# Performance work log

Measured on AMD Instinct MI355X. Metric: run time of the kernel, lower is better.

The kernel has to match this reference:

```python
import jax, jax.numpy as jnp
import numpy as np

V = 50000
E = 500000
D = 128


def setup_inputs() -> dict:
    key = jax.random.key(0)
    k1, k2, k3, k4, k5, k6 = jax.random.split(key, 6)
    edge_feats = jax.random.normal(k1, (E, D), dtype=jnp.float32)
    node_feats = jax.random.normal(k2, (V, 1), dtype=jnp.float32)
    edge_index = jax.random.randint(k3, (2, E), 0, V, dtype=jnp.int64)
    rev_index = jax.random.randint(k4, (E,), 0, E, dtype=jnp.int64)
    # Linear(hidden_dim, hidden_dim, bias=True) params, Kaiming-uniform-ish init
    lim = 1.0 / np.sqrt(D)
    W = jax.random.uniform(k5, (D, D), dtype=jnp.float32, minval=-lim, maxval=lim)
    b = jax.random.uniform(k6, (D,), dtype=jnp.float32, minval=-lim, maxval=lim)
    return {"edge_feats": edge_feats, "node_feats": node_feats, "W": W, "b": b,
            "edge_index": edge_index, "rev_index": rev_index}


def reference(edge_feats, node_feats, W, b, edge_index, rev_index):
    src, dest = edge_index[0], edge_index[1]
    messages = jax.nn.relu(edge_feats)                      # [E, d]
    # scatter-sum messages onto destination nodes
    node_messages = jax.ops.segment_sum(messages, dest, num_segments=node_feats.shape[0])  # [V, d]
    # gather back to edges, subtract reverse-edge message (D-MPNN)
    edge_messages = node_messages[src] - messages[rev_index]  # [E, d]
    # update: Linear (dropout p=0.0 is identity)
    return edge_messages @ W.T + b
```

## Files before the change

kernel.cpp:

```cpp
#include <hip/hip_runtime.h>

#define DD 128
#define TILE_E 64

typedef __attribute__((ext_vector_type(8))) short short8;
typedef __attribute__((ext_vector_type(4))) float f32x4;

__device__ __forceinline__ unsigned short f2bf(float f) {
  unsigned int u = __float_as_uint(f);
  u += 0x7FFF + ((u >> 16) & 1);
  return (unsigned short)(u >> 16);
}


__global__ __launch_bounds__(256) void hist_kernel(
    const int* __restrict__ eidx, int* __restrict__ cnt, int E) {
  int e = blockIdx.x * 256 + threadIdx.x;
  if (e < E) atomicAdd(&cnt[eidx[E + e]], 1);
}

__global__ __launch_bounds__(1024) void scan_kernel(
    const int* __restrict__ cnt, int* __restrict__ off, int* __restrict__ cur, int V) {
  __shared__ int s[1024];
  const int t = threadIdx.x;
  const int chunk = (V + 1023) / 1024;
  const int lo = t * chunk, hi = min(lo + chunk, V);
  int tot = 0;
  for (int v = lo; v < hi; ++v) tot += cnt[v];
  s[t] = tot;
  __syncthreads();
  for (int d = 1; d < 1024; d <<= 1) {
    int x = (t >= d) ? s[t - d] : 0;
    __syncthreads();
    s[t] += x;
    __syncthreads();
  }
  int run = (t > 0) ? s[t - 1] : 0;
  for (int v = lo; v < hi; ++v) {
    off[v] = run; cur[v] = run;
    run += cnt[v];
  }
}

__global__ __launch_bounds__(256) void fill_kernel(
    const int* __restrict__ eidx, int* __restrict__ cur,
    int* __restrict__ elist, int E) {
  int e = blockIdx.x * 256 + threadIdx.x;
  if (e < E) {
    int p = atomicAdd(&cur[eidx[E + e]], 1);
    elist[p] = e;
  }
}

__global__ __launch_bounds__(256) void gather_sum_kernel(
    const float* __restrict__ ef, const int* __restrict__ off,
    const int* __restrict__ cnt, const int* __restrict__ elist,
    float* __restrict__ nm, int V) {
  const int lane = threadIdx.x & 63;
  const int v = blockIdx.x * 4 + (threadIdx.x >> 6);
  if (v >= V) return;
  const int base = off[v];
  const int deg  = cnt[v];
  float2 acc0 = make_float2(0.f, 0.f);
  float2 acc1 = make_float2(0.f, 0.f);
  int j = 0;
  for (; j + 4 <= deg; j += 4) {
    int ea = elist[base + j + 0];
    int eb = elist[base + j + 1];
    int ec = elist[base + j + 2];
    int ed = elist[base + j + 3];
    float2 ma = ((const float2*)(ef + (size_t)ea * DD))[lane];
    float2 mb = ((const float2*)(ef + (size_t)eb * DD))[lane];
    float2 mc = ((const float2*)(ef + (size_t)ec * DD))[lane];
    float2 md = ((const float2*)(ef + (size_t)ed * DD))[lane];
    acc0.x += fmaxf(ma.x, 0.f) + fmaxf(mb.x, 0.f);
    acc0.y += fmaxf(ma.y, 0.f) + fmaxf(mb.y, 0.f);
    acc1.x += fmaxf(mc.x, 0.f) + fmaxf(md.x, 0.f);
    acc1.y += fmaxf(mc.y, 0.f) + fmaxf(md.y, 0.f);
  }
  for (; j < deg; ++j) {
    int e = elist[base + j];
    float2 m = ((const float2*)(ef + (size_t)e * DD))[lane];
    acc0.x += fmaxf(m.x, 0.f);
    acc0.y += fmaxf(m.y, 0.f);
  }
  ((float2*)(nm + (size_t)v * DD))[lane] =
      make_float2(acc0.x + acc1.x, acc0.y + acc1.y);
}

__global__ __launch_bounds__(256) void wconv_kernel(
    const float* __restrict__ W, unsigned short* __restrict__ Wswz) {
  int idx = blockIdx.x * 256 + threadIdx.x;
  if (idx >= DD * DD / 8) return;
  int lane = idx & 63;
  int nt   = (idx >> 6) & 7;
  int kt   = idx >> 9;
  int n = nt * 16 + (lane & 15);
  int k = kt * 32 + (lane >> 4) * 8;
  const float4* wrow = (const float4*)(W + (size_t)n * DD + k);
  float4 w0 = wrow[0];
  float4 w1 = wrow[1];
  unsigned int p0 = f2bf(w0.x) | ((unsigned int)f2bf(w0.y) << 16);
  unsigned int p1 = f2bf(w0.z) | ((unsigned int)f2bf(w0.w) << 16);
  unsigned int p2 = f2bf(w1.x) | ((unsigned int)f2bf(w1.y) << 16);
  unsigned int p3 = f2bf(w1.z) | ((unsigned int)f2bf(w1.w) << 16);
  ((uint4*)Wswz)[idx] = make_uint4(p0, p1, p2, p3);
}

__global__ __launch_bounds__(256, 4) void fused_gather_gemm_kernel(
    const float* __restrict__ ef, const float* __restrict__ nm,
    const unsigned short* __restrict__ Wswz, const float* __restrict__ bias,
    const int* __restrict__ eidx, const int* __restrict__ rev,
    float* __restrict__ out, int E) {
  const int tid  = threadIdx.x;
  const int lane = tid & 63;
  const int wave = tid >> 6;
  const int col  = lane & 15;
  const int quad = lane >> 4;
  const int e0   = blockIdx.x * TILE_E + wave * 16;

  const int ea = e0 + col;
  int s = 0, rv = 0;
  if (ea < E) { s = eidx[ea]; rv = rev[ea]; }
  const float4* __restrict__ nmp = (const float4*)(nm + (size_t)s  * DD);
  const float4* __restrict__ efp = (const float4*)(ef + (size_t)rv * DD);
  const short8* __restrict__ wp  = (const short8*)Wswz + lane;

  f32x4 acc[8];
  #pragma unroll
  for (int i = 0; i < 8; ++i) acc[i] = (f32x4){0.f, 0.f, 0.f, 0.f};

  #pragma unroll
  for (int kt = 0; kt < 4; ++kt) {
    const int k4 = kt * 8 + quad * 2;
    float4 a0 = nmp[k4];
    float4 a1 = nmp[k4 + 1];
    float4 m0 = efp[k4];
    float4 m1 = efp[k4 + 1];
    float x0 = a0.x - fmaxf(m0.x, 0.f);
    float x1 = a0.y - fmaxf(m0.y, 0.f);
    float x2 = a0.z - fmaxf(m0.z, 0.f);
    float x3 = a0.w - fmaxf(m0.w, 0.f);
    float x4 = a1.x - fmaxf(m1.x, 0.f);
    float x5 = a1.y - fmaxf(m1.y, 0.f);
    float x6 = a1.z - fmaxf(m1.z, 0.f);
    float x7 = a1.w - fmaxf(m1.w, 0.f);
    union { unsigned int u[4]; short8 s8; } cvt;
    cvt.u[0] = f2bf(x0) | ((unsigned int)f2bf(x1) << 16);
    cvt.u[1] = f2bf(x2) | ((unsigned int)f2bf(x3) << 16);
    cvt.u[2] = f2bf(x4) | ((unsigned int)f2bf(x5) << 16);
    cvt.u[3] = f2bf(x6) | ((unsigned int)f2bf(x7) << 16);
    short8 a = cvt.s8;
    #pragma unroll
    for (int nt = 0; nt < 8; ++nt) {
      short8 b = wp[(kt * 8 + nt) * 64];
      acc[nt] = __builtin_amdgcn_mfma_f32_16x16x32_bf16(a, b, acc[nt], 0, 0, 0);
    }
  }

  #pragma unroll
  for (int nt = 0; nt < 8; ++nt) {
    float bj = bias[nt * 16 + col];
    #pragma unroll
    for (int r = 0; r < 4; ++r) {
      int e = e0 + quad * 4 + r;
      if (e < E) out[(size_t)e * DD + nt * 16 + col] = acc[nt][r] + bj;
    }
  }
}

extern "C" void kernel_launch(void* const* d_in, const int* in_sizes, int n_in,
                              void* d_out, int out_size, void* d_ws, size_t ws_size,
                              hipStream_t stream) {
  const float* ef   = (const float*)d_in[0];
  const float* W    = (const float*)d_in[2];
  const float* bias = (const float*)d_in[3];
  const int*   eidx = (const int*)d_in[4];
  const int*   rev  = (const int*)d_in[5];
  float*       out  = (float*)d_out;

  const int V = in_sizes[1];
  const int E = in_sizes[5];

  char* ws = (char*)d_ws;
  size_t o = 0;
  float* nm = (float*)(ws + o);            o += (size_t)V * DD * sizeof(float);
  o = (o + 255) & ~(size_t)255;
  int* cnt  = (int*)(ws + o);              o += (size_t)V * sizeof(int);
  o = (o + 255) & ~(size_t)255;
  int* off  = (int*)(ws + o);              o += (size_t)V * sizeof(int);
  o = (o + 255) & ~(size_t)255;
  int* cur  = (int*)(ws + o);              o += (size_t)V * sizeof(int);
  o = (o + 255) & ~(size_t)255;
  int* elist = (int*)(ws + o);             o += (size_t)E * sizeof(int);
  o = (o + 255) & ~(size_t)255;
  unsigned short* Wswz = (unsigned short*)(ws + o);

  hipMemsetAsync(cnt, 0, (size_t)V * sizeof(int), stream);

  int eb = (E + 255) / 256;
  hist_kernel<<<eb, 256, 0, stream>>>(eidx, cnt, E);
  scan_kernel<<<1, 1024, 0, stream>>>(cnt, off, cur, V);
  fill_kernel<<<eb, 256, 0, stream>>>(eidx, cur, elist, E);
  gather_sum_kernel<<<(V + 3) / 4, 256, 0, stream>>>(ef, off, cnt, elist, nm, V);
  wconv_kernel<<<(DD * DD / 8 + 255) / 256, 256, 0, stream>>>(W, Wswz);

  int nblocks = (E + TILE_E - 1) / TILE_E;
  fused_gather_gemm_kernel<<<nblocks, 256, 0, stream>>>(ef, nm, Wswz, bias, eidx, rev, out, E);
}
```

Baseline: 740.2 us.

## Widen gather loads to float4, hoist GEMM operand loads, use nontemporal output stores

The segment-sum kernel now has each half-wave handle a different edge with float4 loads, so one wave reads two 512-byte rows per instruction with eight edges in flight per iteration. The half-wave partial sums are then combined with a cross-half shuffle. The fused gather-GEMM kernel issues all nm and ef row loads up front, before any MFMA, to expose more memory-level parallelism, and writes the output with nontemporal stores to avoid cache pollution. The trade-off is higher register pressure from the hoisted loads, plus the extra shuffle and half-wave divergence in the tail loop.

```diff
diff --git a/kernel.cpp b/kernel.cpp
--- a/kernel.cpp
+++ b/kernel.cpp
@@ -57,35 +57,46 @@
     const int* __restrict__ cnt, const int* __restrict__ elist,
     float* __restrict__ nm, int V) {
   const int lane = threadIdx.x & 63;
+  const int half = lane >> 5;
+  const int l32  = lane & 31;
   const int v = blockIdx.x * 4 + (threadIdx.x >> 6);
   if (v >= V) return;
   const int base = off[v];
   const int deg  = cnt[v];
-  float2 acc0 = make_float2(0.f, 0.f);
-  float2 acc1 = make_float2(0.f, 0.f);
+  f32x4 acc = (f32x4){0.f, 0.f, 0.f, 0.f};
   int j = 0;
-  for (; j + 4 <= deg; j += 4) {
-    int ea = elist[base + j + 0];
-    int eb = elist[base + j + 1];
-    int ec = elist[base + j + 2];
-    int ed = elist[base + j + 3];
-    float2 ma = ((const float2*)(ef + (size_t)ea * DD))[lane];
-    float2 mb = ((const float2*)(ef + (size_t)eb * DD))[lane];
-    float2 mc = ((const float2*)(ef + (size_t)ec * DD))[lane];
-    float2 md = ((const float2*)(ef + (size_t)ed * DD))[lane];
-    acc0.x += fmaxf(ma.x, 0.f) + fmaxf(mb.x, 0.f);
-    acc0.y += fmaxf(ma.y, 0.f) + fmaxf(mb.y, 0.f);
-    acc1.x += fmaxf(mc.x, 0.f) + fmaxf(md.x, 0.f);
-    acc1.y += fmaxf(mc.y, 0.f) + fmaxf(md.y, 0.f);
-  }
-  for (; j < deg; ++j) {
-    int e = elist[base + j];
-    float2 m = ((const float2*)(ef + (size_t)e * DD))[lane];
-    acc0.x += fmaxf(m.x, 0.f);
-    acc0.y += fmaxf(m.y, 0.f);
-  }
-  ((float2*)(nm + (size_t)v * DD))[lane] =
-      make_float2(acc0.x + acc1.x, acc0.y + acc1.y);
+  for (; j + 8 <= deg; j += 8) {
+    int e0 = elist[base + j + 0 + half];
+    int e1 = elist[base + j + 2 + half];
+    int e2 = elist[base + j + 4 + half];
+    int e3 = elist[base + j + 6 + half];
+    float4 m0 = ((const float4*)(ef + (size_t)e0 * DD))[l32];
+    float4 m1 = ((const float4*)(ef + (size_t)e1 * DD))[l32];
+    float4 m2 = ((const float4*)(ef + (size_t)e2 * DD))[l32];
+    float4 m3 = ((const float4*)(ef + (size_t)e3 * DD))[l32];
+    acc[0] += fmaxf(m0.x, 0.f) + fmaxf(m1.x, 0.f) + fmaxf(m2.x, 0.f) + fmaxf(m3.x, 0.f);
+    acc[1] += fmaxf(m0.y, 0.f) + fmaxf(m1.y, 0.f) + fmaxf(m2.y, 0.f) + fmaxf(m3.y, 0.f);
+    acc[2] += fmaxf(m0.z, 0.f) + fmaxf(m1.z, 0.f) + fmaxf(m2.z, 0.f) + fmaxf(m3.z, 0.f);
+    acc[3] += fmaxf(m0.w, 0.f) + fmaxf(m1.w, 0.f) + fmaxf(m2.w, 0.f) + fmaxf(m3.w, 0.f);
+  }
+  for (; j < deg; j += 2) {
+    int idx = j + half;
+    if (idx < deg) {
+      int e = elist[base + idx];
+      float4 m = ((const float4*)(ef + (size_t)e * DD))[l32];
+      acc[0] += fmaxf(m.x, 0.f);
+      acc[1] += fmaxf(m.y, 0.f);
+      acc[2] += fmaxf(m.z, 0.f);
+      acc[3] += fmaxf(m.w, 0.f);
+    }
+  }
+  float4 tot;
+  tot.x = acc[0] + __shfl_xor(acc[0], 32);
+  tot.y = acc[1] + __shfl_xor(acc[1], 32);
+  tot.z = acc[2] + __shfl_xor(acc[2], 32);
+  tot.w = acc[3] + __shfl_xor(acc[3], 32);
+  if (half == 0)
+    ((float4*)(nm + (size_t)v * DD))[l32] = tot;
 }
 
 __global__ __launch_bounds__(256) void wconv_kernel(
@@ -126,17 +137,24 @@
   const float4* __restrict__ efp = (const float4*)(ef + (size_t)rv * DD);
   const short8* __restrict__ wp  = (const short8*)Wswz + lane;
 
-  f32x4 acc[8];
-  #pragma unroll
-  for (int i = 0; i < 8; ++i) acc[i] = (f32x4){0.f, 0.f, 0.f, 0.f};
-
+  float4 a[8], m[8];
   #pragma unroll
   for (int kt = 0; kt < 4; ++kt) {
     const int k4 = kt * 8 + quad * 2;
-    float4 a0 = nmp[k4];
-    float4 a1 = nmp[k4 + 1];
-    float4 m0 = efp[k4];
-    float4 m1 = efp[k4 + 1];
+    a[kt * 2]     = nmp[k4];
+    a[kt * 2 + 1] = nmp[k4 + 1];
+    m[kt * 2]     = efp[k4];
+    m[kt * 2 + 1] = efp[k4 + 1];
+  }
+
+  f32x4 acc[8];
+  #pragma unroll
+  for (int i = 0; i < 8; ++i) acc[i] = (f32x4){0.f, 0.f, 0.f, 0.f};
+
+  #pragma unroll
+  for (int kt = 0; kt < 4; ++kt) {
+    float4 a0 = a[kt * 2], a1 = a[kt * 2 + 1];
+    float4 m0 = m[kt * 2], m1 = m[kt * 2 + 1];
     float x0 = a0.x - fmaxf(m0.x, 0.f);
     float x1 = a0.y - fmaxf(m0.y, 0.f);
     float x2 = a0.z - fmaxf(m0.z, 0.f);
@@ -150,11 +168,11 @@
     cvt.u[1] = f2bf(x2) | ((unsigned int)f2bf(x3) << 16);
     cvt.u[2] = f2bf(x4) | ((unsigned int)f2bf(x5) << 16);
     cvt.u[3] = f2bf(x6) | ((unsigned int)f2bf(x7) << 16);
-    short8 a = cvt.s8;
+    short8 av = cvt.s8;
     #pragma unroll
     for (int nt = 0; nt < 8; ++nt) {
       short8 b = wp[(kt * 8 + nt) * 64];
-      acc[nt] = __builtin_amdgcn_mfma_f32_16x16x32_bf16(a, b, acc[nt], 0, 0, 0);
+      acc[nt] = __builtin_amdgcn_mfma_f32_16x16x32_bf16(av, b, acc[nt], 0, 0, 0);
     }
   }
 
@@ -164,7 +182,9 @@
     #pragma unroll
     for (int r = 0; r < 4; ++r) {
       int e = e0 + quad * 4 + r;
-      if (e < E) out[(size_t)e * DD + nt * 16 + col] = acc[nt][r] + bj;
+      if (e < E)
+        __builtin_nontemporal_store(acc[nt][r] + bj,
+                                    &out[(size_t)e * DD + nt * 16 + col]);
     }
   }
 }
```

Result: no change. 730.2 us (-1.4%).
